# Performance work log

Hardware: AMD Instinct MI355X
Metric: run time of the kernel (lower is better)

The kernel has to match this reference:

```python
import jax, jax.numpy as jnp
import numpy as np

B, H, S, D = 2, 16, 2048, 64
SCALE = 1.0 / (D ** 0.5)
MASK_FILL = -1e9


def setup_inputs() -> dict:
    key = jax.random.key(0)
    kq, kk, kv = jax.random.split(key, 3)
    q = jax.random.normal(kq, (B, H, S, D), dtype=jnp.float32)
    k = jax.random.normal(kk, (B, H, S, D), dtype=jnp.float32)
    v = jax.random.normal(kv, (B, H, S, D), dtype=jnp.float32)
    # causal mask: True where attention is disallowed (j > i)
    attn_mask = jnp.triu(jnp.ones((S, S), dtype=jnp.bool_), k=1)[None, None]
    return {"q": q, "k": k, "v": v, "attn_mask": attn_mask}


def reference(q, k, v, attn_mask):
    # scores: [B,H,S,S] = (q @ k^T) * scale, then masked_fill(mask, -1e9)
    scores = jnp.einsum("bhqd,bhkd->bhqk", q, k) * SCALE
    scores = jnp.where(attn_mask, MASK_FILL, scores)
    attn_prob = jax.nn.softmax(scores, axis=-1)  # dropout p=0.0 (eval)
    context = jnp.einsum("bhqk,bhkd->bhqd", attn_prob, v)
    return (context, attn_prob)
```

## Files before the change

### kernel.cpp

```cpp
#include <hip/hip_runtime.h>

#define NB 2
#define NH 16
#define SS 2048
#define DD 64
constexpr float kScale = 0.125f;

typedef __attribute__((ext_vector_type(8))) short bf16x8;
typedef __attribute__((ext_vector_type(4))) float f32x4;

union FragAB { bf16x8 v; unsigned u[4]; };

__device__ __forceinline__ unsigned pack2bf(float lo, float hi) {
  unsigned ul = __float_as_uint(lo) + 0x8000u;
  unsigned uh = __float_as_uint(hi) + 0x8000u;
  return __builtin_amdgcn_perm(uh, ul, 0x07060302u);
}
__device__ __forceinline__ short f2bf(float f) {
  return (short)((__float_as_uint(f) + 0x8000u) >> 16);
}

struct KC { float4 x[8]; };

__global__ __launch_bounds__(256, 4) void attn_mfma(
    const float* __restrict__ Q, const float* __restrict__ K,
    const float* __restrict__ V, float* __restrict__ ctx,
    float* __restrict__ prob) {
  const int b    = blockIdx.x;
  const int xcd  = b & 7;
  const int slot = b >> 3;
  const int oct  = slot >> 5;
  const int cu5  = slot & 31;
  const int ww   = cu5 & 7;
  const int hl   = cu5 >> 3;
  const int qt   = (3 - oct) * 8 + ((oct & 1) ? (7 - ww) : ww);
  const int bh   = xcd * 4 + hl;

  const int t    = threadIdx.x;
  const int lane = t & 63;
  const int wave = t >> 6;
  const int quad = lane >> 4;
  const int l16  = lane & 15;

  const int q_base = qt * 64;
  const int i_max  = q_base + 63;
  const int qw     = q_base + wave * 16;
  const size_t hoff = (size_t)bh * SS * DD;
  const float* Kh = K + hoff;
  const float* Vh = V + hoff;

  __shared__ __align__(16) short Vt[2][DD][40];
  __shared__ __align__(16) short Pld[4][16][40];
  __shared__ float linv_s[4][20];

  FragAB aq[2];
  {
    const float* qp = Q + hoff + (size_t)(qw + l16) * DD + quad * 8;
#pragma unroll
    for (int c = 0; c < 2; ++c) {
      float4 x = *(const float4*)(qp + c * 32);
      float4 y = *(const float4*)(qp + c * 32 + 4);
      aq[c].u[0] = pack2bf(x.x * kScale, x.y * kScale);
      aq[c].u[1] = pack2bf(x.z * kScale, x.w * kScale);
      aq[c].u[2] = pack2bf(y.x * kScale, y.y * kScale);
      aq[c].u[3] = pack2bf(y.z * kScale, y.w * kScale);
    }
  }

  const int irow0 = qw + quad * 4;
  const int nc = (i_max + 32) >> 5;

  auto kload = [&](KC& kk, int j0) {
    const float* kp = Kh + (size_t)(j0 + l16) * DD + quad * 8;
    kk.x[0] = *(const float4*)(kp);
    kk.x[1] = *(const float4*)(kp + 4);
    kk.x[2] = *(const float4*)(kp + 32);
    kk.x[3] = *(const float4*)(kp + 36);
    kk.x[4] = *(const float4*)(kp + 16 * DD);
    kk.x[5] = *(const float4*)(kp + 16 * DD + 4);
    kk.x[6] = *(const float4*)(kp + 16 * DD + 32);
    kk.x[7] = *(const float4*)(kp + 16 * DD + 36);
  };

  auto qke = [&](const KC& kk, int j0, f32x4 et[2]) {
#pragma unroll
    for (int tl = 0; tl < 2; ++tl) {
      const float4 a  = kk.x[tl * 4 + 0];
      const float4 b2 = kk.x[tl * 4 + 1];
      const float4 cc = kk.x[tl * 4 + 2];
      const float4 d2 = kk.x[tl * 4 + 3];
      FragAB b0, b1;
      b0.u[0] = pack2bf(a.x, a.y);   b0.u[1] = pack2bf(a.z, a.w);
      b0.u[2] = pack2bf(b2.x, b2.y); b0.u[3] = pack2bf(b2.z, b2.w);
      b1.u[0] = pack2bf(cc.x, cc.y); b1.u[1] = pack2bf(cc.z, cc.w);
      b1.u[2] = pack2bf(d2.x, d2.y); b1.u[3] = pack2bf(d2.z, d2.w);
      f32x4 acc = {0.f, 0.f, 0.f, 0.f};
      acc = __builtin_amdgcn_mfma_f32_16x16x32_bf16(aq[0].v, b0.v, acc, 0, 0, 0);
      acc = __builtin_amdgcn_mfma_f32_16x16x32_bf16(aq[1].v, b1.v, acc, 0, 0, 0);
      const int jc = j0 + tl * 16 + l16;
#pragma unroll
      for (int r = 0; r < 4; ++r)
        et[tl][r] = (jc <= irow0 + r) ? __expf(acc[r]) : 0.f;
    }
  };

  const int jj = t >> 3;
  const int d0 = (t & 7) * 8;
  const int cw = jj ^ ((t & 3) << 3);

  f32x4 O[4] = {{0,0,0,0},{0,0,0,0},{0,0,0,0},{0,0,0,0}};
  float l_acc[4] = {0.f, 0.f, 0.f, 0.f};

  {
    const float* vp = Vh + (size_t)jj * DD + d0;
    float4 pv0 = *(const float4*)vp, pv1 = *(const float4*)(vp + 4);
    float tmp[8] = {pv0.x,pv0.y,pv0.z,pv0.w,pv1.x,pv1.y,pv1.z,pv1.w};
#pragma unroll
    for (int i2 = 0; i2 < 8; ++i2) Vt[0][d0 + i2][cw] = f2bf(tmp[i2]);
  }

  KC ka, kb;
  kload(ka, 0);

  auto body = [&](int c, const KC& kc, KC& kn, bool pf) {
    __syncthreads();
    const int cn = c + 1;
    float4 pv0, pv1;
    if (cn < nc) {
      const float* vp = Vh + (size_t)(cn * 32 + jj) * DD + d0;
      pv0 = *(const float4*)vp; pv1 = *(const float4*)(vp + 4);
    }
    if (pf) kload(kn, cn * 32);
    f32x4 et[2];
    qke(kc, c * 32, et);
#pragma unroll
    for (int r = 0; r < 4; ++r) l_acc[r] += et[0][r] + et[1][r];
#pragma unroll
    for (int tl = 0; tl < 2; ++tl)
#pragma unroll
      for (int r = 0; r < 4; ++r)
        Pld[wave][quad * 4 + r][tl * 16 + l16] = f2bf(et[tl][r]);
    FragAB ap;
    ap.v = *(const bf16x8*)&Pld[wave][l16][quad * 8];
    const int vb = c & 1;
#pragma unroll
    for (int n = 0; n < 4; ++n) {
      const int dim = n * 16 + l16;
      const int cb = (quad << 3) ^ ((((dim >> 3) & 3)) << 3);
      FragAB bv;
      bv.v = *(const bf16x8*)&Vt[vb][dim][cb];
      O[n] = __builtin_amdgcn_mfma_f32_16x16x32_bf16(ap.v, bv.v, O[n], 0, 0, 0);
    }
    if (cn < nc) {
      float tmp[8] = {pv0.x,pv0.y,pv0.z,pv0.w,pv1.x,pv1.y,pv1.z,pv1.w};
#pragma unroll
      for (int i2 = 0; i2 < 8; ++i2) Vt[cn & 1][d0 + i2][cw] = f2bf(tmp[i2]);
    }
  };

  {
    int c = 0;
    for (; c + 2 <= nc; c += 2) {
      body(c, ka, kb, true);
      body(c + 1, kb, ka, c + 2 < nc);
    }
  }

  float inv_l[4];
#pragma unroll
  for (int r = 0; r < 4; ++r) {
    float s2 = l_acc[r];
    s2 += __shfl_xor(s2, 1, 64);
    s2 += __shfl_xor(s2, 2, 64);
    s2 += __shfl_xor(s2, 4, 64);
    s2 += __shfl_xor(s2, 8, 64);
    inv_l[r] = 1.f / s2;
  }
  if (l16 < 4) linv_s[wave][quad * 4 + l16] = inv_l[l16];

#pragma unroll
  for (int n = 0; n < 4; ++n)
#pragma unroll
    for (int r = 0; r < 4; ++r)
      __builtin_nontemporal_store(
          O[n][r] * inv_l[r],
          ctx + (size_t)(bh * SS + irow0 + r) * DD + n * 16 + l16);

  const float lv = linv_s[wave][l16];
  float* pr2 = prob + (size_t)(bh * SS + qw + l16) * SS;

  kload(ka, 0);
  for (int c = 0; c < nc; c += 2) {
    kload(kb, (c + 1) * 32);
#pragma unroll
    for (int h = 0; h < 2; ++h) {
      const KC& kc = h ? kb : ka;
      const int cc2 = c + h;
      if (h == 1 && cc2 + 1 < nc) kload(ka, (cc2 + 1) * 32);
      f32x4 et[2];
      qke(kc, cc2 * 32, et);
#pragma unroll
      for (int tl = 0; tl < 2; ++tl)
#pragma unroll
        for (int r = 0; r < 4; ++r)
          Pld[wave][quad * 4 + r][tl * 16 + l16] = f2bf(et[tl][r]);
      FragAB ap;
      ap.v = *(const bf16x8*)&Pld[wave][l16][quad * 8];
      f32x4 o0, o1;
      o0[0] = __uint_as_float(ap.u[0] << 16) * lv;
      o0[1] = __uint_as_float(ap.u[0] & 0xffff0000u) * lv;
      o0[2] = __uint_as_float(ap.u[1] << 16) * lv;
      o0[3] = __uint_as_float(ap.u[1] & 0xffff0000u) * lv;
      o1[0] = __uint_as_float(ap.u[2] << 16) * lv;
      o1[1] = __uint_as_float(ap.u[2] & 0xffff0000u) * lv;
      o1[2] = __uint_as_float(ap.u[3] << 16) * lv;
      o1[3] = __uint_as_float(ap.u[3] & 0xffff0000u) * lv;
      __builtin_nontemporal_store(o0, (f32x4*)(pr2 + cc2 * 32 + quad * 8));
      __builtin_nontemporal_store(o1, (f32x4*)(pr2 + cc2 * 32 + quad * 8 + 4));
    }
  }

  const f32x4 z4 = {0.f, 0.f, 0.f, 0.f};
  for (int c = nc; c < SS / 32; ++c) {
    __builtin_nontemporal_store(z4, (f32x4*)(pr2 + c * 32 + quad * 8));
    __builtin_nontemporal_store(z4, (f32x4*)(pr2 + c * 32 + quad * 8 + 4));
  }
}

extern "C" void kernel_launch(void* const* d_in, const int* in_sizes, int n_in,
                              void* d_out, int out_size, void* d_ws, size_t ws_size,
                              hipStream_t stream) {
  const float* q = (const float*)d_in[0];
  const float* k = (const float*)d_in[1];
  const float* v = (const float*)d_in[2];
  float* ctx  = (float*)d_out;
  float* prob = (float*)d_out + (size_t)NB * NH * SS * DD;
  attn_mfma<<<dim3(NB * NH * 32), dim3(256), 0, stream>>>(q, k, v, ctx, prob);
}
```

Measured before the change: 819.7 us.

## Split key range across two wave groups per block and combine partial sums

Blocks grow to 512 threads, and two groups of four waves each handle alternating 32-key chunks for the same 64 query rows. The partial O and row-sum accumulators are merged through a shared-memory union after the first pass. The probability pass is also split by chunk parity and now stores probabilities straight from registers instead of round-tripping through LDS. The aim is to shorten the serial chunk loop and raise per-block parallelism, at the cost of an LDS combine step, extra barriers and more register pressure under the 512,8 launch bounds.

```diff
diff --git a/kernel.cpp b/kernel.cpp
--- a/kernel.cpp
+++ b/kernel.cpp
@@ -22,7 +22,18 @@
 
 struct KC { float4 x[8]; };
 
-__global__ __launch_bounds__(256, 4) void attn_mfma(
+struct P1 {
+  short Vt[2][2][DD][40];
+  short Pld[8][16][40];
+};
+struct Comb {
+  float Osum[4][16][DD];
+  float lsum[4][16];
+  float linv[64];
+};
+union SMemU { P1 p1; Comb comb; };
+
+__global__ __launch_bounds__(512, 8) void attn_mfma(
     const float* __restrict__ Q, const float* __restrict__ K,
     const float* __restrict__ V, float* __restrict__ ctx,
     float* __restrict__ prob) {
@@ -39,19 +50,19 @@
   const int t    = threadIdx.x;
   const int lane = t & 63;
   const int wave = t >> 6;
+  const int w3   = wave & 3;
+  const int g    = wave >> 2;
   const int quad = lane >> 4;
   const int l16  = lane & 15;
 
   const int q_base = qt * 64;
   const int i_max  = q_base + 63;
-  const int qw     = q_base + wave * 16;
+  const int qw     = q_base + w3 * 16;
   const size_t hoff = (size_t)bh * SS * DD;
   const float* Kh = K + hoff;
   const float* Vh = V + hoff;
 
-  __shared__ __align__(16) short Vt[2][DD][40];
-  __shared__ __align__(16) short Pld[4][16][40];
-  __shared__ float linv_s[4][20];
+  __shared__ __align__(16) SMemU sm;
 
   FragAB aq[2];
   {
@@ -69,6 +80,7 @@
 
   const int irow0 = qw + quad * 4;
   const int nc = (i_max + 32) >> 5;
+  const int iters = nc >> 1;
 
   auto kload = [&](KC& kk, int j0) {
     const float* kp = Kh + (size_t)(j0 + l16) * DD + quad * 8;
@@ -104,69 +116,74 @@
     }
   };
 
-  const int jj = t >> 3;
-  const int d0 = (t & 7) * 8;
-  const int cw = jj ^ ((t & 3) << 3);
+  const int tg = t & 255;
+  const int jj = tg >> 3;
+  const int d0 = (tg & 7) * 8;
+  const int cw = jj ^ ((tg & 3) << 3);
 
   f32x4 O[4] = {{0,0,0,0},{0,0,0,0},{0,0,0,0},{0,0,0,0}};
   float l_acc[4] = {0.f, 0.f, 0.f, 0.f};
 
   {
-    const float* vp = Vh + (size_t)jj * DD + d0;
+    const float* vp = Vh + (size_t)(g * 32 + jj) * DD + d0;
     float4 pv0 = *(const float4*)vp, pv1 = *(const float4*)(vp + 4);
     float tmp[8] = {pv0.x,pv0.y,pv0.z,pv0.w,pv1.x,pv1.y,pv1.z,pv1.w};
 #pragma unroll
-    for (int i2 = 0; i2 < 8; ++i2) Vt[0][d0 + i2][cw] = f2bf(tmp[i2]);
-  }
-
-  KC ka, kb;
-  kload(ka, 0);
-
-  auto body = [&](int c, const KC& kc, KC& kn, bool pf) {
+    for (int i2 = 0; i2 < 8; ++i2) sm.p1.Vt[g][0][d0 + i2][cw] = f2bf(tmp[i2]);
+  }
+
+  KC k0, k1;
+  kload(k0, g * 32);
+
+  auto p1body = [&](int it, const KC& cur, KC& nxt) {
+    const int c = 2 * it + g;
     __syncthreads();
-    const int cn = c + 1;
+    const bool more = (it + 1) < iters;
     float4 pv0, pv1;
-    if (cn < nc) {
-      const float* vp = Vh + (size_t)(cn * 32 + jj) * DD + d0;
+    if (more) {
+      const float* vp = Vh + (size_t)((c + 2) * 32 + jj) * DD + d0;
       pv0 = *(const float4*)vp; pv1 = *(const float4*)(vp + 4);
-    }
-    if (pf) kload(kn, cn * 32);
+      kload(nxt, (c + 2) * 32);
+    }
     f32x4 et[2];
-    qke(kc, c * 32, et);
+    qke(cur, c * 32, et);
 #pragma unroll
     for (int r = 0; r < 4; ++r) l_acc[r] += et[0][r] + et[1][r];
 #pragma unroll
     for (int tl = 0; tl < 2; ++tl)
 #pragma unroll
       for (int r = 0; r < 4; ++r)
-        Pld[wave][quad * 4 + r][tl * 16 + l16] = f2bf(et[tl][r]);
+        sm.p1.Pld[wave][quad * 4 + r][tl * 16 + l16] = f2bf(et[tl][r]);
     FragAB ap;
-    ap.v = *(const bf16x8*)&Pld[wave][l16][quad * 8];
-    const int vb = c & 1;
+    ap.v = *(const bf16x8*)&sm.p1.Pld[wave][l16][quad * 8];
+    const int vb = it & 1;
 #pragma unroll
     for (int n = 0; n < 4; ++n) {
       const int dim = n * 16 + l16;
       const int cb = (quad << 3) ^ ((((dim >> 3) & 3)) << 3);
       FragAB bv;
-      bv.v = *(const bf16x8*)&Vt[vb][dim][cb];
+      bv.v = *(const bf16x8*)&sm.p1.Vt[g][vb][dim][cb];
       O[n] = __builtin_amdgcn_mfma_f32_16x16x32_bf16(ap.v, bv.v, O[n], 0, 0, 0);
     }
-    if (cn < nc) {
+    if (more) {
       float tmp[8] = {pv0.x,pv0.y,pv0.z,pv0.w,pv1.x,pv1.y,pv1.z,pv1.w};
 #pragma unroll
-      for (int i2 = 0; i2 < 8; ++i2) Vt[cn & 1][d0 + i2][cw] = f2bf(tmp[i2]);
-    }
-  };
-
-  {
-    int c = 0;
-    for (; c + 2 <= nc; c += 2) {
-      body(c, ka, kb, true);
-      body(c + 1, kb, ka, c + 2 < nc);
-    }
-  }
-
-  float inv_l[4];
+      for (int i2 = 0; i2 < 8; ++i2)
+        sm.p1.Vt[g][vb ^ 1][d0 + i2][cw] = f2bf(tmp[i2]);
+    }
+  };
+
+  {
+    int it = 0;
+    while (true) {
+      p1body(it, k0, k1);
+      if (++it == iters) break;
+      p1body(it, k1, k0);
+      if (++it == iters) break;
+    }
+  }
+
+  float lrow[4];
 #pragma unroll
   for (int r = 0; r < 4; ++r) {
     float s2 = l_acc[r];
@@ -174,56 +191,71 @@
     s2 += __shfl_xor(s2, 2, 64);
     s2 += __shfl_xor(s2, 4, 64);
     s2 += __shfl_xor(s2, 8, 64);
-    inv_l[r] = 1.f / s2;
-  }
-  if (l16 < 4) linv_s[wave][quad * 4 + l16] = inv_l[l16];
-
-#pragma unroll
-  for (int n = 0; n < 4; ++n)
+    lrow[r] = s2;
+  }
+
+  __syncthreads();
+  if (g == 1) {
+#pragma unroll
+    for (int n = 0; n < 4; ++n)
+#pragma unroll
+      for (int r = 0; r < 4; ++r)
+        sm.comb.Osum[w3][quad * 4 + r][n * 16 + l16] = O[n][r];
+    if (l16 < 4) sm.comb.lsum[w3][quad * 4 + l16] = lrow[l16];
+  }
+  __syncthreads();
+  if (g == 0) {
+    float inv_l[4];
 #pragma unroll
     for (int r = 0; r < 4; ++r)
-      __builtin_nontemporal_store(
-          O[n][r] * inv_l[r],
-          ctx + (size_t)(bh * SS + irow0 + r) * DD + n * 16 + l16);
-
-  const float lv = linv_s[wave][l16];
-  float* pr2 = prob + (size_t)(bh * SS + qw + l16) * SS;
-
-  kload(ka, 0);
-  for (int c = 0; c < nc; c += 2) {
-    kload(kb, (c + 1) * 32);
-#pragma unroll
-    for (int h = 0; h < 2; ++h) {
-      const KC& kc = h ? kb : ka;
-      const int cc2 = c + h;
-      if (h == 1 && cc2 + 1 < nc) kload(ka, (cc2 + 1) * 32);
-      f32x4 et[2];
-      qke(kc, cc2 * 32, et);
-#pragma unroll
-      for (int tl = 0; tl < 2; ++tl)
-#pragma unroll
-        for (int r = 0; r < 4; ++r)
-          Pld[wave][quad * 4 + r][tl * 16 + l16] = f2bf(et[tl][r]);
-      FragAB ap;
-      ap.v = *(const bf16x8*)&Pld[wave][l16][quad * 8];
-      f32x4 o0, o1;
-      o0[0] = __uint_as_float(ap.u[0] << 16) * lv;
-      o0[1] = __uint_as_float(ap.u[0] & 0xffff0000u) * lv;
-      o0[2] = __uint_as_float(ap.u[1] << 16) * lv;
-      o0[3] = __uint_as_float(ap.u[1] & 0xffff0000u) * lv;
-      o1[0] = __uint_as_float(ap.u[2] << 16) * lv;
-      o1[1] = __uint_as_float(ap.u[2] & 0xffff0000u) * lv;
-      o1[2] = __uint_as_float(ap.u[3] << 16) * lv;
-      o1[3] = __uint_as_float(ap.u[3] & 0xffff0000u) * lv;
-      __builtin_nontemporal_store(o0, (f32x4*)(pr2 + cc2 * 32 + quad * 8));
-      __builtin_nontemporal_store(o1, (f32x4*)(pr2 + cc2 * 32 + quad * 8 + 4));
-    }
-  }
-
+      inv_l[r] = 1.f / (lrow[r] + sm.comb.lsum[w3][quad * 4 + r]);
+#pragma unroll
+    for (int n = 0; n < 4; ++n)
+#pragma unroll
+      for (int r = 0; r < 4; ++r)
+        O[n][r] += sm.comb.Osum[w3][quad * 4 + r][n * 16 + l16];
+    if (l16 < 4) sm.comb.linv[w3 * 16 + quad * 4 + l16] = inv_l[l16];
+#pragma unroll
+    for (int n = 0; n < 4; ++n)
+#pragma unroll
+      for (int r = 0; r < 4; ++r)
+        __builtin_nontemporal_store(
+            O[n][r] * inv_l[r],
+            ctx + (size_t)(bh * SS + irow0 + r) * DD + n * 16 + l16);
+  }
+  __syncthreads();
+  float inv2[4];
+#pragma unroll
+  for (int r = 0; r < 4; ++r) inv2[r] = sm.comb.linv[w3 * 16 + quad * 4 + r];
+
+  auto p2body = [&](int c, const KC& cur, KC& nxt) {
+    if (c + 2 < nc) kload(nxt, (c + 2) * 32);
+    f32x4 et[2];
+    qke(cur, c * 32, et);
+#pragma unroll
+    for (int tl = 0; tl < 2; ++tl)
+#pragma unroll
+      for (int r = 0; r < 4; ++r)
+        __builtin_nontemporal_store(
+            et[tl][r] * inv2[r],
+            prob + (size_t)(bh * SS + irow0 + r) * SS + c * 32 + tl * 16 + l16);
+  };
+  {
+    kload(k0, g * 32);
+    int c = g;
+    while (true) {
+      p2body(c, k0, k1);
+      c += 2; if (c >= nc) break;
+      p2body(c, k1, k0);
+      c += 2; if (c >= nc) break;
+    }
+  }
+
+  float* prz = prob + (size_t)(bh * SS + qw + l16) * SS;
   const f32x4 z4 = {0.f, 0.f, 0.f, 0.f};
-  for (int c = nc; c < SS / 32; ++c) {
-    __builtin_nontemporal_store(z4, (f32x4*)(pr2 + c * 32 + quad * 8));
-    __builtin_nontemporal_store(z4, (f32x4*)(pr2 + c * 32 + quad * 8 + 4));
+  for (int z = nc + g; z < SS / 32; z += 2) {
+    __builtin_nontemporal_store(z4, (f32x4*)(prz + z * 32 + quad * 8));
+    __builtin_nontemporal_store(z4, (f32x4*)(prz + z * 32 + quad * 8 + 4));
   }
 }
 
@@ -235,5 +267,5 @@
   const float* v = (const float*)d_in[2];
   float* ctx  = (float*)d_out;
   float* prob = (float*)d_out + (size_t)NB * NH * SS * DD;
-  attn_mfma<<<dim3(NB * NH * 32), dim3(256), 0, stream>>>(q, k, v, ctx, prob);
-}
+  attn_mfma<<<dim3(NB * NH * 32), dim3(512), 0, stream>>>(q, k, v, ctx, prob);
+}
```

New measurement: 1.557 ms. +90.0%, slower.

## Make each wave iterate its own causal extent with per-wave V staging

Applied to the files above, without the earlier changes.

Each wave now loops over 16-key steps only up to its own 16-row causal limit, rather than the whole 64-row block's extent, so it skips fully masked tiles. V is staged into a per-wave LDS buffer, which removes the block-wide __syncthreads. The probability pass now writes fp32 exp values scaled by inv_l directly from registers, without the LDS bf16 round trip. Zero-fill of the masked region is reorganised into row-wise vector stores. The risks are scalar 4-byte prob stores, which coalesce less well than the previous 16-byte stores, and four times the V staging work, since every wave converts its own copy.

```diff
diff --git a/kernel.cpp b/kernel.cpp
--- a/kernel.cpp
+++ b/kernel.cpp
@@ -20,7 +20,8 @@
   return (short)((__float_as_uint(f) + 0x8000u) >> 16);
 }
 
-struct KC { float4 x[8]; };
+struct KC { float4 x[4]; };
+struct VC { float4 x[4]; };
 
 __global__ __launch_bounds__(256, 4) void attn_mfma(
     const float* __restrict__ Q, const float* __restrict__ K,
@@ -42,16 +43,13 @@
   const int quad = lane >> 4;
   const int l16  = lane & 15;
 
-  const int q_base = qt * 64;
-  const int i_max  = q_base + 63;
-  const int qw     = q_base + wave * 16;
+  const int qw   = qt * 64 + wave * 16;
   const size_t hoff = (size_t)bh * SS * DD;
   const float* Kh = K + hoff;
   const float* Vh = V + hoff;
 
-  __shared__ __align__(16) short Vt[2][DD][40];
+  __shared__ __align__(16) short Vt[4][DD][40];
   __shared__ __align__(16) short Pld[4][16][40];
-  __shared__ float linv_s[4][20];
 
   FragAB aq[2];
   {
@@ -68,102 +66,87 @@
   }
 
   const int irow0 = qw + quad * 4;
-  const int nc = (i_max + 32) >> 5;
-
-  auto kload = [&](KC& kk, int j0) {
-    const float* kp = Kh + (size_t)(j0 + l16) * DD + quad * 8;
+  const int ns = ((((qw + 15) >> 4) + 1) + 1) & ~1;
+
+  auto kload = [&](KC& kk, int s) {
+    const float* kp = Kh + (size_t)(s * 16 + l16) * DD + quad * 8;
     kk.x[0] = *(const float4*)(kp);
     kk.x[1] = *(const float4*)(kp + 4);
     kk.x[2] = *(const float4*)(kp + 32);
     kk.x[3] = *(const float4*)(kp + 36);
-    kk.x[4] = *(const float4*)(kp + 16 * DD);
-    kk.x[5] = *(const float4*)(kp + 16 * DD + 4);
-    kk.x[6] = *(const float4*)(kp + 16 * DD + 32);
-    kk.x[7] = *(const float4*)(kp + 16 * DD + 36);
-  };
-
-  auto qke = [&](const KC& kk, int j0, f32x4 et[2]) {
-#pragma unroll
-    for (int tl = 0; tl < 2; ++tl) {
-      const float4 a  = kk.x[tl * 4 + 0];
-      const float4 b2 = kk.x[tl * 4 + 1];
-      const float4 cc = kk.x[tl * 4 + 2];
-      const float4 d2 = kk.x[tl * 4 + 3];
-      FragAB b0, b1;
-      b0.u[0] = pack2bf(a.x, a.y);   b0.u[1] = pack2bf(a.z, a.w);
-      b0.u[2] = pack2bf(b2.x, b2.y); b0.u[3] = pack2bf(b2.z, b2.w);
-      b1.u[0] = pack2bf(cc.x, cc.y); b1.u[1] = pack2bf(cc.z, cc.w);
-      b1.u[2] = pack2bf(d2.x, d2.y); b1.u[3] = pack2bf(d2.z, d2.w);
-      f32x4 acc = {0.f, 0.f, 0.f, 0.f};
-      acc = __builtin_amdgcn_mfma_f32_16x16x32_bf16(aq[0].v, b0.v, acc, 0, 0, 0);
-      acc = __builtin_amdgcn_mfma_f32_16x16x32_bf16(aq[1].v, b1.v, acc, 0, 0, 0);
-      const int jc = j0 + tl * 16 + l16;
-#pragma unroll
-      for (int r = 0; r < 4; ++r)
-        et[tl][r] = (jc <= irow0 + r) ? __expf(acc[r]) : 0.f;
-    }
-  };
-
-  const int jj = t >> 3;
-  const int d0 = (t & 7) * 8;
-  const int cw = jj ^ ((t & 3) << 3);
+  };
+  auto qke = [&](const KC& kk, int s, f32x4& et) {
+    FragAB b0, b1;
+    b0.u[0] = pack2bf(kk.x[0].x, kk.x[0].y);
+    b0.u[1] = pack2bf(kk.x[0].z, kk.x[0].w);
+    b0.u[2] = pack2bf(kk.x[1].x, kk.x[1].y);
+    b0.u[3] = pack2bf(kk.x[1].z, kk.x[1].w);
+    b1.u[0] = pack2bf(kk.x[2].x, kk.x[2].y);
+    b1.u[1] = pack2bf(kk.x[2].z, kk.x[2].w);
+    b1.u[2] = pack2bf(kk.x[3].x, kk.x[3].y);
+    b1.u[3] = pack2bf(kk.x[3].z, kk.x[3].w);
+    f32x4 acc = {0.f, 0.f, 0.f, 0.f};
+    acc = __builtin_amdgcn_mfma_f32_16x16x32_bf16(aq[0].v, b0.v, acc, 0, 0, 0);
+    acc = __builtin_amdgcn_mfma_f32_16x16x32_bf16(aq[1].v, b1.v, acc, 0, 0, 0);
+    const int jc = s * 16 + l16;
+#pragma unroll
+    for (int r = 0; r < 4; ++r)
+      et[r] = (jc <= irow0 + r) ? __expf(acc[r]) : 0.f;
+  };
+
+  const int vp2 = lane >> 3;
+  const int vdq = (lane & 7) * 8;
+  const int vswz = (((vdq >> 3) & 3) << 3);
+  auto vload = [&](VC& vv, int s) {
+    const float* vp = Vh + (size_t)(s * 16 + vp2 * 2) * DD + vdq;
+    vv.x[0] = *(const float4*)(vp);
+    vv.x[1] = *(const float4*)(vp + 4);
+    vv.x[2] = *(const float4*)(vp + DD);
+    vv.x[3] = *(const float4*)(vp + DD + 4);
+  };
+  auto vstage = [&](const VC& vv, int s) {
+    const int col = ((s & 1) * 16 + vp2 * 2) ^ vswz;
+    const float* a  = (const float*)&vv.x[0];
+    const float* bq = (const float*)&vv.x[2];
+#pragma unroll
+    for (int i = 0; i < 8; ++i)
+      *(unsigned*)&Vt[wave][vdq + i][col] = pack2bf(a[i], bq[i]);
+  };
 
   f32x4 O[4] = {{0,0,0,0},{0,0,0,0},{0,0,0,0},{0,0,0,0}};
   float l_acc[4] = {0.f, 0.f, 0.f, 0.f};
 
-  {
-    const float* vp = Vh + (size_t)jj * DD + d0;
-    float4 pv0 = *(const float4*)vp, pv1 = *(const float4*)(vp + 4);
-    float tmp[8] = {pv0.x,pv0.y,pv0.z,pv0.w,pv1.x,pv1.y,pv1.z,pv1.w};
-#pragma unroll
-    for (int i2 = 0; i2 < 8; ++i2) Vt[0][d0 + i2][cw] = f2bf(tmp[i2]);
-  }
-
-  KC ka, kb;
-  kload(ka, 0);
-
-  auto body = [&](int c, const KC& kc, KC& kn, bool pf) {
-    __syncthreads();
-    const int cn = c + 1;
-    float4 pv0, pv1;
-    if (cn < nc) {
-      const float* vp = Vh + (size_t)(cn * 32 + jj) * DD + d0;
-      pv0 = *(const float4*)vp; pv1 = *(const float4*)(vp + 4);
+  KC k0, k1;
+  VC vr;
+  kload(k0, 0);
+  vload(vr, 0);
+  vstage(vr, 0);
+
+  for (int s = 0; s < ns; ++s) {
+    const bool more = (s + 1) < ns;
+    KC& kc = (s & 1) ? k1 : k0;
+    KC& kn = (s & 1) ? k0 : k1;
+    if (more) { kload(kn, s + 1); vload(vr, s + 1); }
+    f32x4 et;
+    qke(kc, s, et);
+#pragma unroll
+    for (int r = 0; r < 4; ++r) l_acc[r] += et[r];
+#pragma unroll
+    for (int r = 0; r < 4; ++r)
+      Pld[wave][quad * 4 + r][(s & 1) * 16 + l16] = f2bf(et[r]);
+    if (s & 1) {
+      FragAB ap;
+      ap.v = *(const bf16x8*)&Pld[wave][l16][quad * 8];
+#pragma unroll
+      for (int n = 0; n < 4; ++n) {
+        const int dim = n * 16 + l16;
+        const int cb = (quad << 3) ^ (((dim >> 3) & 3) << 3);
+        FragAB bv;
+        bv.v = *(const bf16x8*)&Vt[wave][dim][cb];
+        O[n] = __builtin_amdgcn_mfma_f32_16x16x32_bf16(ap.v, bv.v, O[n], 0, 0, 0);
+      }
     }
-    if (pf) kload(kn, cn * 32);
-    f32x4 et[2];
-    qke(kc, c * 32, et);
-#pragma unroll
-    for (int r = 0; r < 4; ++r) l_acc[r] += et[0][r] + et[1][r];
-#pragma unroll
-    for (int tl = 0; tl < 2; ++tl)
-#pragma unroll
-      for (int r = 0; r < 4; ++r)
-        Pld[wave][quad * 4 + r][tl * 16 + l16] = f2bf(et[tl][r]);
-    FragAB ap;
-    ap.v = *(const bf16x8*)&Pld[wave][l16][quad * 8];
-    const int vb = c & 1;
-#pragma unroll
-    for (int n = 0; n < 4; ++n) {
-      const int dim = n * 16 + l16;
-      const int cb = (quad << 3) ^ ((((dim >> 3) & 3)) << 3);
-      FragAB bv;
-      bv.v = *(const bf16x8*)&Vt[vb][dim][cb];
-      O[n] = __builtin_amdgcn_mfma_f32_16x16x32_bf16(ap.v, bv.v, O[n], 0, 0, 0);
-    }
-    if (cn < nc) {
-      float tmp[8] = {pv0.x,pv0.y,pv0.z,pv0.w,pv1.x,pv1.y,pv1.z,pv1.w};
-#pragma unroll
-      for (int i2 = 0; i2 < 8; ++i2) Vt[cn & 1][d0 + i2][cw] = f2bf(tmp[i2]);
-    }
-  };
-
-  {
-    int c = 0;
-    for (; c + 2 <= nc; c += 2) {
-      body(c, ka, kb, true);
-      body(c + 1, kb, ka, c + 2 < nc);
-    }
+    if (more) vstage(vr, s + 1);
   }
 
   float inv_l[4];
@@ -176,7 +159,6 @@
     s2 += __shfl_xor(s2, 8, 64);
     inv_l[r] = 1.f / s2;
   }
-  if (l16 < 4) linv_s[wave][quad * 4 + l16] = inv_l[l16];
 
 #pragma unroll
   for (int n = 0; n < 4; ++n)
@@ -186,44 +168,28 @@
           O[n][r] * inv_l[r],
           ctx + (size_t)(bh * SS + irow0 + r) * DD + n * 16 + l16);
 
-  const float lv = linv_s[wave][l16];
-  float* pr2 = prob + (size_t)(bh * SS + qw + l16) * SS;
-
-  kload(ka, 0);
-  for (int c = 0; c < nc; c += 2) {
-    kload(kb, (c + 1) * 32);
-#pragma unroll
-    for (int h = 0; h < 2; ++h) {
-      const KC& kc = h ? kb : ka;
-      const int cc2 = c + h;
-      if (h == 1 && cc2 + 1 < nc) kload(ka, (cc2 + 1) * 32);
-      f32x4 et[2];
-      qke(kc, cc2 * 32, et);
-#pragma unroll
-      for (int tl = 0; tl < 2; ++tl)
-#pragma unroll
-        for (int r = 0; r < 4; ++r)
-          Pld[wave][quad * 4 + r][tl * 16 + l16] = f2bf(et[tl][r]);
-      FragAB ap;
-      ap.v = *(const bf16x8*)&Pld[wave][l16][quad * 8];
-      f32x4 o0, o1;
-      o0[0] = __uint_as_float(ap.u[0] << 16) * lv;
-      o0[1] = __uint_as_float(ap.u[0] & 0xffff0000u) * lv;
-      o0[2] = __uint_as_float(ap.u[1] << 16) * lv;
-      o0[3] = __uint_as_float(ap.u[1] & 0xffff0000u) * lv;
-      o1[0] = __uint_as_float(ap.u[2] << 16) * lv;
-      o1[1] = __uint_as_float(ap.u[2] & 0xffff0000u) * lv;
-      o1[2] = __uint_as_float(ap.u[3] << 16) * lv;
-      o1[3] = __uint_as_float(ap.u[3] & 0xffff0000u) * lv;
-      __builtin_nontemporal_store(o0, (f32x4*)(pr2 + cc2 * 32 + quad * 8));
-      __builtin_nontemporal_store(o1, (f32x4*)(pr2 + cc2 * 32 + quad * 8 + 4));
-    }
-  }
-
+  kload(k0, 0);
+  for (int s = 0; s < ns; ++s) {
+    const bool more = (s + 1) < ns;
+    KC& kc = (s & 1) ? k1 : k0;
+    KC& kn = (s & 1) ? k0 : k1;
+    if (more) kload(kn, s + 1);
+    f32x4 et;
+    qke(kc, s, et);
+#pragma unroll
+    for (int r = 0; r < 4; ++r)
+      __builtin_nontemporal_store(
+          et[r] * inv_l[r],
+          prob + (size_t)(bh * SS + irow0 + r) * SS + s * 16 + l16);
+  }
+
+  const int zc0 = ns * 16;
+  float* pzb = prob + (size_t)(bh * SS + qw) * SS;
   const f32x4 z4 = {0.f, 0.f, 0.f, 0.f};
-  for (int c = nc; c < SS / 32; ++c) {
-    __builtin_nontemporal_store(z4, (f32x4*)(pr2 + c * 32 + quad * 8));
-    __builtin_nontemporal_store(z4, (f32x4*)(pr2 + c * 32 + quad * 8 + 4));
+  for (int r = 0; r < 16; ++r) {
+    float* pz = pzb + (size_t)r * SS;
+    for (int zb = zc0 + lane * 4; zb < SS; zb += 256)
+      __builtin_nontemporal_store(z4, (f32x4*)(pz + zb));
   }
 }
 
```

New measurement: 1.249 ms. 52.4% more time.
